# Kernel optimization log

Measured on AMD Instinct MI355X. Metric: run time of the kernel, lower is better.

Reference implementation:

```python
import jax, jax.numpy as jnp
import numpy as np

B, T, I, H = 4, 128, 32, 64


def setup_inputs() -> dict:
    key = jax.random.key(0)
    k1, k2, k3 = jax.random.split(key, 3)
    x = jax.random.normal(k1, (B, T, I), dtype=jnp.float32)
    carry = jnp.zeros((B, H), dtype=jnp.float32)  # RNNCell.initialize_carry uses zeros
    # lecun_normal-like input kernel (default_kernel_init)
    Wi = jax.random.normal(k2, (I, H), dtype=jnp.float32) / np.float32(np.sqrt(I))
    # orthogonal recurrent kernel init
    Wh, _ = jnp.linalg.qr(jax.random.normal(k3, (H, H), dtype=jnp.float32))
    b = jnp.zeros((H,), dtype=jnp.float32)
    return {"carry": carry, "x": x, "Wi": Wi, "Wh": Wh, "b": b}


def reference(carry, x, Wi, Wh, b):
    # Vanilla RNN step: a = tanh(x_t @ Wi + h @ Wh + b), scanned over time (axis 1).
    # Per step we also emit the analytic forward-mode Jacobian of the new state
    # w.r.t. (Wi, Wh, b, carry) -- exactly what jacfwd(fn, argnums=(0,1)) computes.
    Hh = Wh.shape[0]
    Bb = carry.shape[0]
    eyeH = jnp.eye(Hh, dtype=x.dtype)
    eyeB = jnp.eye(Bb, dtype=x.dtype)

    def step(h, x_t):
        a = jnp.tanh(x_t @ Wi + h @ Wh + b)  # (B, H)
        g = 1.0 - a * a                      # tanh' at preactivation, (B, H)
        # d a[b,j] / d Wi[i,k] = g[b,j] * x[b,i] * delta(j,k)  -> (B, H, I, H)
        J_Wi = jnp.einsum('bj,bi,jk->bjik', g, x_t, eyeH)
        # d a[b,j] / d Wh[m,k] = g[b,j] * h[b,m] * delta(j,k)  -> (B, H, H, H)
        J_Wh = jnp.einsum('bj,bm,jk->bjmk', g, h, eyeH)
        # d a[b,j] / d b[k]    = g[b,j] * delta(j,k)           -> (B, H, H)
        J_b = jnp.einsum('bj,jk->bjk', g, eyeH)
        # d a[b,j] / d h[c,m]  = g[b,j] * Wh[m,j] * delta(b,c) -> (B, H, B, H)
        J_h = jnp.einsum('bj,mj,bc->bjcm', g, Wh, eyeB)
        return a, (a, J_Wi, J_Wh, J_b, J_h)

    final_carry, ys = jax.lax.scan(step, carry, jnp.moveaxis(x, 1, 0))
    # out_axes=1: time axis goes to position 1 of every output leaf
    out, J_Wi, J_Wh, J_b, J_h = jax.tree.map(lambda y: jnp.moveaxis(y, 0, 1), ys)
    return final_carry, out, J_Wi, J_Wh, J_b, J_h
```

## Files before the change

kernel.cpp:

```cpp
#include <hip/hip_runtime.h>
#include <math.h>

#define OFF_OUT   256u
#define OFF_JWI   33024u
#define OFF_JWH   67141888u
#define OFF_JB    201359616u
#define OFF_JH    203456768u

typedef float f32x4 __attribute__((ext_vector_type(4)));

static __device__ __forceinline__ float tanh_fast(float x) {
    float t = __expf(2.0f * x);
    return 1.0f - 2.0f / (t + 1.0f);
}

static __device__ __forceinline__ void nt_store4(f32x4* p, float a, float b,
                                                 float c, float d) {
    f32x4 r = {a, b, c, d};
    __builtin_nontemporal_store(r, p);
}

__global__ __launch_bounds__(256) void xwi_kernel(
    const float* __restrict__ x, const float* __restrict__ Wi,
    const float* __restrict__ bias, float* __restrict__ u)
{
    const int tid = threadIdx.x;
    const int row = blockIdx.x * 4 + (tid >> 6);
    const int j = tid & 63;
    const float* xr = x + row * 32;
    float acc = bias[j];
#pragma unroll
    for (int i = 0; i < 32; ++i) acc = fmaf(xr[i], Wi[i * 64 + j], acc);
    u[row * 64 + j] = acc;
}

__global__ __launch_bounds__(64) void scan_kernel(
    const float* __restrict__ carry, const float* __restrict__ u,
    const float* __restrict__ Wh, float* __restrict__ out)
{
    const int b = blockIdx.x;
    const int j = threadIdx.x;
    float wcol[64];
#pragma unroll
    for (int m = 0; m < 64; ++m) wcol[m] = Wh[m * 64 + j];

    __shared__ float sh[64];
    sh[j] = carry[b * 64 + j];
    const float* ub = u + b * 128 * 64;
    float* ob = out + OFF_OUT + b * 128 * 64;
    float unext = ub[j];
    float a = 0.0f;
    __syncthreads();

    for (int t = 0; t < 128; ++t) {
        const float pre0 = unext;
        if (t < 127) unext = ub[(t + 1) * 64 + j];
        float a0 = 0.f, a1 = 0.f, a2 = 0.f, a3 = 0.f;
#pragma unroll
        for (int m = 0; m < 64; m += 4) {
            a0 = fmaf(sh[m + 0], wcol[m + 0], a0);
            a1 = fmaf(sh[m + 1], wcol[m + 1], a1);
            a2 = fmaf(sh[m + 2], wcol[m + 2], a2);
            a3 = fmaf(sh[m + 3], wcol[m + 3], a3);
        }
        a = tanh_fast(pre0 + (a0 + a1) + (a2 + a3));
        ob[t * 64 + j] = a;
        __syncthreads();
        sh[j] = a;
        __syncthreads();
    }
    out[b * 64 + j] = a;
}

__global__ __launch_bounds__(256) void fill_main(
    const float* __restrict__ carry, const float* __restrict__ x,
    float* __restrict__ out)
{
    __shared__ float smem[1024];
    const int tid = threadIdx.x;
    const unsigned blk = blockIdx.x;
    const float* __restrict__ outh = out + OFF_OUT;
    const unsigned rowq = tid >> 4;
    const unsigned k0 = (tid & 15u) * 4;

    if (blk < 1024u) {
        const unsigned bt = blk >> 1, jh = blk & 1u;
        if (tid < 32) {
            const float aa = outh[bt * 64 + jh * 32 + tid];
            smem[tid] = 1.0f - aa * aa;
            smem[32 + tid] = x[bt * 32 + tid];
        }
        __syncthreads();
        f32x4* dst = reinterpret_cast<f32x4*>(
            out + (size_t)OFF_JWI + (size_t)bt * 131072 + jh * 65536);
        const unsigned jbase = jh * 32;
#pragma unroll 2
        for (int it = 0; it < 64; ++it) {
            const unsigned R = it * 16 + rowq;
            const unsigned jloc = R >> 5, i = R & 31u;
            const float val = smem[jloc] * smem[32 + i];
            const unsigned d = (jbase + jloc) - k0;
            nt_store4(dst + it * 256 + tid,
                      (d == 0u) ? val : 0.f, (d == 1u) ? val : 0.f,
                      (d == 2u) ? val : 0.f, (d == 3u) ? val : 0.f);
        }
    } else if (blk < 3072u) {
        const unsigned idx = blk - 1024u;
        const unsigned bt = idx >> 2, jq = idx & 3u;
        const unsigned t = bt & 127u, bb = bt >> 7;
        if (tid < 16) {
            const float aa = outh[bt * 64 + jq * 16 + tid];
            smem[tid] = 1.0f - aa * aa;
        } else if (tid >= 64 && tid < 128) {
            const unsigned m = tid - 64;
            smem[64 + m] = (t == 0u) ? carry[bb * 64 + m]
                                     : outh[(bt - 1u) * 64 + m];
        }
        __syncthreads();
        f32x4* dst = reinterpret_cast<f32x4*>(
            out + (size_t)OFF_JWH + (size_t)bt * 262144 + jq * 65536);
        const unsigned jbase = jq * 16;
#pragma unroll 2
        for (int it = 0; it < 64; ++it) {
            const unsigned R = it * 16 + rowq;
            const unsigned jloc = R >> 6, m = R & 63u;
            const float val = smem[jloc] * smem[64 + m];
            const unsigned d = (jbase + jloc) - k0;
            nt_store4(dst + it * 256 + tid,
                      (d == 0u) ? val : 0.f, (d == 1u) ? val : 0.f,
                      (d == 2u) ? val : 0.f, (d == 3u) ? val : 0.f);
        }
    } else {
        const unsigned c = blk - 3072u;
        for (int p = tid; p < 1024; p += 256) {
            const float aa = outh[c * 1024 + p];
            smem[p] = 1.0f - aa * aa;
        }
        __syncthreads();
        f32x4* dst = reinterpret_cast<f32x4*>(
            out + (size_t)OFF_JB + (size_t)c * 65536);
#pragma unroll 2
        for (int it = 0; it < 64; ++it) {
            const unsigned R = it * 16 + rowq;
            const unsigned j = R & 63u;
            const float val = smem[R];
            const unsigned d = j - k0;
            nt_store4(dst + it * 256 + tid,
                      (d == 0u) ? val : 0.f, (d == 1u) ? val : 0.f,
                      (d == 2u) ? val : 0.f, (d == 3u) ? val : 0.f);
        }
    }
}

__global__ __launch_bounds__(256) void fill_jh(
    const float* __restrict__ Wh, float* __restrict__ out)
{
    __shared__ float whT[64 * 68];
    __shared__ float sg[256];
    const int tid = threadIdx.x;
    const unsigned q = blockIdx.x;
    const float* __restrict__ outh = out + OFF_OUT;

    for (int p = tid; p < 4096; p += 256) {
        const unsigned m = p >> 6, j = p & 63u;
        whT[j * 68 + m] = Wh[p];
    }
    {
        const unsigned s = tid >> 6, j = tid & 63u;
        const float aa = outh[(q * 4 + s) * 64 + j];
        sg[tid] = 1.0f - aa * aa;
    }
    __syncthreads();

    const unsigned m0 = (tid & 15u) * 4;
    f32x4* dst = reinterpret_cast<f32x4*>(out + (size_t)OFF_JH + (size_t)q * 65536);
#pragma unroll 2
    for (int it = 0; it < 64; ++it) {
        const unsigned R = it * 16 + (tid >> 4);
        const unsigned s = R >> 8;
        const unsigned j = (R >> 2) & 63u;
        const unsigned cc = R & 3u;
        const unsigned bb = (q * 4 + s) >> 7;
        if (cc == bb) {
            const float g = sg[s * 64 + j];
            const float* wrow = &whT[j * 68 + m0];
            nt_store4(dst + it * 256 + tid,
                      g * wrow[0], g * wrow[1], g * wrow[2], g * wrow[3]);
        } else {
            nt_store4(dst + it * 256 + tid, 0.f, 0.f, 0.f, 0.f);
        }
    }
}

extern "C" void kernel_launch(void* const* d_in, const int* in_sizes, int n_in,
                              void* d_out, int out_size, void* d_ws, size_t ws_size,
                              hipStream_t stream) {
    const float* carry = (const float*)d_in[0];
    const float* x     = (const float*)d_in[1];
    const float* Wi    = (const float*)d_in[2];
    const float* Wh    = (const float*)d_in[3];
    const float* bias  = (const float*)d_in[4];
    float* out = (float*)d_out;
    float* u = out + OFF_JB;

    xwi_kernel <<<128, 256, 0, stream>>>(x, Wi, bias, u);
    scan_kernel<<<4, 64, 0, stream>>>(carry, u, Wh, out);
    fill_main  <<<3104, 256, 0, stream>>>(carry, x, out);
    fill_jh    <<<128, 256, 0, stream>>>(Wh, out);
}
```

Baseline: 206.7 us.

## Overlap serial RNN scan with zero-filling of off-diagonal Jacobian blocks

The scan now runs in block 0 of a combined kernel, with one wavefront per batch row. It drops the per-step __syncthreads and relies on each wavefront executing in lockstep over its own shared-memory slice. The remaining blocks of that kernel write zeros to the halves of J_Wi, J_Wh and J_h that can never hold a nonzero, so that bandwidth-bound traffic overlaps the latency-bound recurrence. A second grid-stride kernel then writes only the diagonal-bearing parts of all four Jacobians, merging the former fill_main and fill_jh into one launch. The risk is that the barrier-free recurrence depends on wavefront-synchronous LDS ordering, and that the zero-fill now competes with the scan for the GPU.

```diff
diff --git a/kernel.cpp b/kernel.cpp
--- a/kernel.cpp
+++ b/kernel.cpp
@@ -14,12 +14,6 @@
     return 1.0f - 2.0f / (t + 1.0f);
 }
 
-static __device__ __forceinline__ void nt_store4(f32x4* p, float a, float b,
-                                                 float c, float d) {
-    f32x4 r = {a, b, c, d};
-    __builtin_nontemporal_store(r, p);
-}
-
 __global__ __launch_bounds__(256) void xwi_kernel(
     const float* __restrict__ x, const float* __restrict__ Wi,
     const float* __restrict__ bias, float* __restrict__ u)
@@ -34,161 +28,128 @@
     u[row * 64 + j] = acc;
 }
 
-__global__ __launch_bounds__(64) void scan_kernel(
+__global__ __launch_bounds__(256) void scan_zero_kernel(
     const float* __restrict__ carry, const float* __restrict__ u,
     const float* __restrict__ Wh, float* __restrict__ out)
 {
-    const int b = blockIdx.x;
-    const int j = threadIdx.x;
-    float wcol[64];
+    const int tid = threadIdx.x;
+    if (blockIdx.x == 0) {
+        const int w = tid >> 6, j = tid & 63;
+        float wcol[64];
 #pragma unroll
-    for (int m = 0; m < 64; ++m) wcol[m] = Wh[m * 64 + j];
-
-    __shared__ float sh[64];
-    sh[j] = carry[b * 64 + j];
-    const float* ub = u + b * 128 * 64;
-    float* ob = out + OFF_OUT + b * 128 * 64;
-    float unext = ub[j];
-    float a = 0.0f;
-    __syncthreads();
-
-    for (int t = 0; t < 128; ++t) {
-        const float pre0 = unext;
-        if (t < 127) unext = ub[(t + 1) * 64 + j];
-        float a0 = 0.f, a1 = 0.f, a2 = 0.f, a3 = 0.f;
+        for (int m = 0; m < 64; ++m) wcol[m] = Wh[m * 64 + j];
+        __shared__ __align__(16) float sh[256];
+        sh[tid] = carry[tid];
+        const float* ub = u + w * 8192;
+        float* ob = out + OFF_OUT + w * 8192;
+        const f32x4* shv = reinterpret_cast<const f32x4*>(sh + w * 64);
+        float unext = ub[j];
+        float a = 0.0f;
+        for (int t = 0; t < 128; ++t) {
+            const float pre = unext;
+            if (t < 127) unext = ub[(t + 1) * 64 + j];
+            float a0 = 0.f, a1 = 0.f, a2 = 0.f, a3 = 0.f;
 #pragma unroll
-        for (int m = 0; m < 64; m += 4) {
-            a0 = fmaf(sh[m + 0], wcol[m + 0], a0);
-            a1 = fmaf(sh[m + 1], wcol[m + 1], a1);
-            a2 = fmaf(sh[m + 2], wcol[m + 2], a2);
-            a3 = fmaf(sh[m + 3], wcol[m + 3], a3);
+            for (int mm = 0; mm < 16; ++mm) {
+                const f32x4 hv = shv[mm];
+                a0 = fmaf(hv.x, wcol[mm * 4 + 0], a0);
+                a1 = fmaf(hv.y, wcol[mm * 4 + 1], a1);
+                a2 = fmaf(hv.z, wcol[mm * 4 + 2], a2);
+                a3 = fmaf(hv.w, wcol[mm * 4 + 3], a3);
+            }
+            a = tanh_fast(pre + (a0 + a1) + (a2 + a3));
+            ob[t * 64 + j] = a;
+            sh[tid] = a;
         }
-        a = tanh_fast(pre0 + (a0 + a1) + (a2 + a3));
-        ob[t * 64 + j] = a;
-        __syncthreads();
-        sh[j] = a;
-        __syncthreads();
-    }
-    out[b * 64 + j] = a;
-}
-
-__global__ __launch_bounds__(256) void fill_main(
-    const float* __restrict__ carry, const float* __restrict__ x,
-    float* __restrict__ out)
-{
-    __shared__ float smem[1024];
-    const int tid = threadIdx.x;
-    const unsigned blk = blockIdx.x;
-    const float* __restrict__ outh = out + OFF_OUT;
-    const unsigned rowq = tid >> 4;
-    const unsigned k0 = (tid & 15u) * 4;
-
-    if (blk < 1024u) {
-        const unsigned bt = blk >> 1, jh = blk & 1u;
-        if (tid < 32) {
-            const float aa = outh[bt * 64 + jh * 32 + tid];
-            smem[tid] = 1.0f - aa * aa;
-            smem[32 + tid] = x[bt * 32 + tid];
-        }
-        __syncthreads();
-        f32x4* dst = reinterpret_cast<f32x4*>(
-            out + (size_t)OFF_JWI + (size_t)bt * 131072 + jh * 65536);
-        const unsigned jbase = jh * 32;
-#pragma unroll 2
-        for (int it = 0; it < 64; ++it) {
-            const unsigned R = it * 16 + rowq;
-            const unsigned jloc = R >> 5, i = R & 31u;
-            const float val = smem[jloc] * smem[32 + i];
-            const unsigned d = (jbase + jloc) - k0;
-            nt_store4(dst + it * 256 + tid,
-                      (d == 0u) ? val : 0.f, (d == 1u) ? val : 0.f,
-                      (d == 2u) ? val : 0.f, (d == 3u) ? val : 0.f);
-        }
-    } else if (blk < 3072u) {
-        const unsigned idx = blk - 1024u;
-        const unsigned bt = idx >> 2, jq = idx & 3u;
-        const unsigned t = bt & 127u, bb = bt >> 7;
-        if (tid < 16) {
-            const float aa = outh[bt * 64 + jq * 16 + tid];
-            smem[tid] = 1.0f - aa * aa;
-        } else if (tid >= 64 && tid < 128) {
-            const unsigned m = tid - 64;
-            smem[64 + m] = (t == 0u) ? carry[bb * 64 + m]
-                                     : outh[(bt - 1u) * 64 + m];
-        }
-        __syncthreads();
-        f32x4* dst = reinterpret_cast<f32x4*>(
-            out + (size_t)OFF_JWH + (size_t)bt * 262144 + jq * 65536);
-        const unsigned jbase = jq * 16;
-#pragma unroll 2
-        for (int it = 0; it < 64; ++it) {
-            const unsigned R = it * 16 + rowq;
-            const unsigned jloc = R >> 6, m = R & 63u;
-            const float val = smem[jloc] * smem[64 + m];
-            const unsigned d = (jbase + jloc) - k0;
-            nt_store4(dst + it * 256 + tid,
-                      (d == 0u) ? val : 0.f, (d == 1u) ? val : 0.f,
-                      (d == 2u) ? val : 0.f, (d == 3u) ? val : 0.f);
-        }
+        out[tid] = a;
     } else {
-        const unsigned c = blk - 3072u;
-        for (int p = tid; p < 1024; p += 256) {
-            const float aa = outh[c * 1024 + p];
-            smem[p] = 1.0f - aa * aa;
-        }
-        __syncthreads();
-        f32x4* dst = reinterpret_cast<f32x4*>(
-            out + (size_t)OFF_JB + (size_t)c * 65536);
-#pragma unroll 2
-        for (int it = 0; it < 64; ++it) {
-            const unsigned R = it * 16 + rowq;
-            const unsigned j = R & 63u;
-            const float val = smem[R];
-            const unsigned d = j - k0;
-            nt_store4(dst + it * 256 + tid,
-                      (d == 0u) ? val : 0.f, (d == 1u) ? val : 0.f,
-                      (d == 2u) ? val : 0.f, (d == 3u) ? val : 0.f);
+        const unsigned NW = (gridDim.x - 1u) * 4u;
+        const unsigned l = tid & 63u;
+        const f32x4 z = {0.f, 0.f, 0.f, 0.f};
+        for (unsigned uu = (blockIdx.x - 1u) * 4u + (tid >> 6);
+             uu < 425984u; uu += NW) {
+            unsigned addr;
+            if (uu < 131072u) {
+                const unsigned r0 = uu * 8u;
+                const unsigned j = (r0 >> 5) & 63u;
+                addr = OFF_JWI + r0 * 64u + ((j < 32u) ? 32u : 0u)
+                     + (l >> 3) * 64u + (l & 7u) * 4u;
+            } else if (uu < 393216u) {
+                const unsigned r0 = (uu - 131072u) * 8u;
+                const unsigned j = (r0 >> 6) & 63u;
+                addr = OFF_JWH + r0 * 64u + ((j < 32u) ? 32u : 0u)
+                     + (l >> 3) * 64u + (l & 7u) * 4u;
+            } else {
+                addr = OFF_JH + (uu - 393216u) * 256u + l * 4u;
+            }
+            __builtin_nontemporal_store(z, reinterpret_cast<f32x4*>(out + addr));
         }
     }
 }
 
-__global__ __launch_bounds__(256) void fill_jh(
+__global__ __launch_bounds__(256) void diag_fill_kernel(
+    const float* __restrict__ carry, const float* __restrict__ x,
     const float* __restrict__ Wh, float* __restrict__ out)
 {
-    __shared__ float whT[64 * 68];
-    __shared__ float sg[256];
     const int tid = threadIdx.x;
-    const unsigned q = blockIdx.x;
+    const unsigned NW = gridDim.x * 4u;
+    const unsigned l = tid & 63u;
     const float* __restrict__ outh = out + OFF_OUT;
 
-    for (int p = tid; p < 4096; p += 256) {
-        const unsigned m = p >> 6, j = p & 63u;
-        whT[j * 68 + m] = Wh[p];
-    }
-    {
-        const unsigned s = tid >> 6, j = tid & 63u;
-        const float aa = outh[(q * 4 + s) * 64 + j];
-        sg[tid] = 1.0f - aa * aa;
-    }
-    __syncthreads();
-
-    const unsigned m0 = (tid & 15u) * 4;
-    f32x4* dst = reinterpret_cast<f32x4*>(out + (size_t)OFF_JH + (size_t)q * 65536);
-#pragma unroll 2
-    for (int it = 0; it < 64; ++it) {
-        const unsigned R = it * 16 + (tid >> 4);
-        const unsigned s = R >> 8;
-        const unsigned j = (R >> 2) & 63u;
-        const unsigned cc = R & 3u;
-        const unsigned bb = (q * 4 + s) >> 7;
-        if (cc == bb) {
-            const float g = sg[s * 64 + j];
-            const float* wrow = &whT[j * 68 + m0];
-            nt_store4(dst + it * 256 + tid,
-                      g * wrow[0], g * wrow[1], g * wrow[2], g * wrow[3]);
+    for (unsigned uu = blockIdx.x * 4u + (tid >> 6); uu < 409600u; uu += NW) {
+        unsigned addr;
+        f32x4 r = {0.f, 0.f, 0.f, 0.f};
+        if (uu < 131072u) {
+            const unsigned r0 = uu * 8u;
+            const unsigned bt = r0 >> 11;
+            const unsigned j = (r0 >> 5) & 63u;
+            const float a = outh[bt * 64u + j];
+            const float g = 1.0f - a * a;
+            const unsigned i = (r0 + (l >> 3)) & 31u;
+            const float v = g * x[bt * 32u + i];
+            const unsigned d = (j & 31u) - (l & 7u) * 4u;
+            r.x = (d == 0u) ? v : 0.f; r.y = (d == 1u) ? v : 0.f;
+            r.z = (d == 2u) ? v : 0.f; r.w = (d == 3u) ? v : 0.f;
+            addr = OFF_JWI + r0 * 64u + ((j < 32u) ? 0u : 32u)
+                 + (l >> 3) * 64u + (l & 7u) * 4u;
+        } else if (uu < 393216u) {
+            const unsigned r0 = (uu - 131072u) * 8u;
+            const unsigned bt = r0 >> 12;
+            const unsigned j = (r0 >> 6) & 63u;
+            const unsigned t = bt & 127u, b = bt >> 7;
+            const float a = outh[bt * 64u + j];
+            const float g = 1.0f - a * a;
+            const unsigned m = (r0 + (l >> 3)) & 63u;
+            const float hv = (t == 0u) ? carry[b * 64u + m]
+                                       : outh[(bt - 1u) * 64u + m];
+            const float v = g * hv;
+            const unsigned d = (j & 31u) - (l & 7u) * 4u;
+            r.x = (d == 0u) ? v : 0.f; r.y = (d == 1u) ? v : 0.f;
+            r.z = (d == 2u) ? v : 0.f; r.w = (d == 3u) ? v : 0.f;
+            addr = OFF_JWH + r0 * 64u + ((j < 32u) ? 0u : 32u)
+                 + (l >> 3) * 64u + (l & 7u) * 4u;
+        } else if (uu < 401408u) {
+            const unsigned p = (uu - 393216u) * 4u + (l >> 4);
+            const unsigned j = p & 63u;
+            const float a = outh[p];
+            const float g = 1.0f - a * a;
+            const unsigned d = j - (l & 15u) * 4u;
+            r.x = (d == 0u) ? g : 0.f; r.y = (d == 1u) ? g : 0.f;
+            r.z = (d == 2u) ? g : 0.f; r.w = (d == 3u) ? g : 0.f;
+            addr = OFF_JB + p * 64u + (l & 15u) * 4u;
         } else {
-            nt_store4(dst + it * 256 + tid, 0.f, 0.f, 0.f, 0.f);
+            const unsigned p = (uu - 401408u) * 4u + (l >> 4);
+            const unsigned bt = p >> 6, j = p & 63u, b = bt >> 7;
+            const float a = outh[p];
+            const float g = 1.0f - a * a;
+            const unsigned k0 = (l & 15u) * 4u;
+            r.x = g * Wh[(k0 + 0u) * 64u + j];
+            r.y = g * Wh[(k0 + 1u) * 64u + j];
+            r.z = g * Wh[(k0 + 2u) * 64u + j];
+            r.w = g * Wh[(k0 + 3u) * 64u + j];
+            addr = OFF_JH + p * 256u + b * 64u + k0;
         }
+        __builtin_nontemporal_store(r, reinterpret_cast<f32x4*>(out + addr));
     }
 }
 
@@ -203,8 +164,7 @@
     float* out = (float*)d_out;
     float* u = out + OFF_JB;
 
-    xwi_kernel <<<128, 256, 0, stream>>>(x, Wi, bias, u);
-    scan_kernel<<<4, 64, 0, stream>>>(carry, u, Wh, out);
-    fill_main  <<<3104, 256, 0, stream>>>(carry, x, out);
-    fill_jh    <<<128, 256, 0, stream>>>(Wh, out);
+    xwi_kernel      <<<128, 256, 0, stream>>>(x, Wi, bias, u);
+    scan_zero_kernel<<<2048, 256, 0, stream>>>(carry, u, Wh, out);
+    diag_fill_kernel<<<2048, 256, 0, stream>>>(carry, x, Wh, out);
 }
```

Measured after the change: 184.4 us. -10.8%, faster.

## Merge fill kernels, stage scan inputs in LDS and drop scan barriers

Applied to the files above, without the earlier changes.

Merges the J_h fill into the main fill kernel, giving one launch and one grid that covers all Jacobian outputs, and moves the J_Wh blocks to the front of the grid. The scan kernel now preloads the whole per-batch preactivation sequence into LDS, keeps the input projection in the out buffer, reads the hidden state as vectors and removes both __syncthreads per step, relying on the 64-thread block being a single wavefront. This targets launch overhead and the barrier latency on the serial recurrence. Without barriers, correctness depends on lockstep wavefront execution, and the block-level fill needs more shared memory.

```diff
diff --git a/kernel.cpp b/kernel.cpp
--- a/kernel.cpp
+++ b/kernel.cpp
@@ -6,6 +6,7 @@
 #define OFF_JWH   67141888u
 #define OFF_JB    201359616u
 #define OFF_JH    203456768u
+#define OUT_TOTAL 211845376u
 
 typedef float f32x4 __attribute__((ext_vector_type(4)));
 
@@ -14,15 +15,9 @@
     return 1.0f - 2.0f / (t + 1.0f);
 }
 
-static __device__ __forceinline__ void nt_store4(f32x4* p, float a, float b,
-                                                 float c, float d) {
-    f32x4 r = {a, b, c, d};
-    __builtin_nontemporal_store(r, p);
-}
-
 __global__ __launch_bounds__(256) void xwi_kernel(
     const float* __restrict__ x, const float* __restrict__ Wi,
-    const float* __restrict__ bias, float* __restrict__ u)
+    const float* __restrict__ bias, float* __restrict__ out)
 {
     const int tid = threadIdx.x;
     const int row = blockIdx.x * 4 + (tid >> 6);
@@ -31,82 +26,60 @@
     float acc = bias[j];
 #pragma unroll
     for (int i = 0; i < 32; ++i) acc = fmaf(xr[i], Wi[i * 64 + j], acc);
-    u[row * 64 + j] = acc;
+    out[OFF_OUT + row * 64 + j] = acc;
 }
 
 __global__ __launch_bounds__(64) void scan_kernel(
-    const float* __restrict__ carry, const float* __restrict__ u,
-    const float* __restrict__ Wh, float* __restrict__ out)
+    const float* __restrict__ carry, const float* __restrict__ Wh,
+    float* __restrict__ out)
 {
     const int b = blockIdx.x;
     const int j = threadIdx.x;
+    __shared__ __align__(16) float uL[128 * 64];
+    __shared__ __align__(16) float sh[64];
+
     float wcol[64];
 #pragma unroll
     for (int m = 0; m < 64; ++m) wcol[m] = Wh[m * 64 + j];
 
-    __shared__ float sh[64];
+    float* ub = out + OFF_OUT + b * 8192;
+#pragma unroll 4
+    for (int p = j; p < 8192; p += 64) uL[p] = ub[p];
     sh[j] = carry[b * 64 + j];
-    const float* ub = u + b * 128 * 64;
-    float* ob = out + OFF_OUT + b * 128 * 64;
-    float unext = ub[j];
+
+    const f32x4* shv = reinterpret_cast<const f32x4*>(sh);
     float a = 0.0f;
-    __syncthreads();
-
     for (int t = 0; t < 128; ++t) {
-        const float pre0 = unext;
-        if (t < 127) unext = ub[(t + 1) * 64 + j];
+        const float pre = uL[t * 64 + j];
         float a0 = 0.f, a1 = 0.f, a2 = 0.f, a3 = 0.f;
 #pragma unroll
-        for (int m = 0; m < 64; m += 4) {
-            a0 = fmaf(sh[m + 0], wcol[m + 0], a0);
-            a1 = fmaf(sh[m + 1], wcol[m + 1], a1);
-            a2 = fmaf(sh[m + 2], wcol[m + 2], a2);
-            a3 = fmaf(sh[m + 3], wcol[m + 3], a3);
+        for (int mm = 0; mm < 16; ++mm) {
+            const f32x4 hv = shv[mm];
+            a0 = fmaf(hv.x, wcol[mm * 4 + 0], a0);
+            a1 = fmaf(hv.y, wcol[mm * 4 + 1], a1);
+            a2 = fmaf(hv.z, wcol[mm * 4 + 2], a2);
+            a3 = fmaf(hv.w, wcol[mm * 4 + 3], a3);
         }
-        a = tanh_fast(pre0 + (a0 + a1) + (a2 + a3));
-        ob[t * 64 + j] = a;
-        __syncthreads();
+        a = tanh_fast(pre + (a0 + a1) + (a2 + a3));
+        ub[t * 64 + j] = a;
         sh[j] = a;
-        __syncthreads();
     }
     out[b * 64 + j] = a;
 }
 
-__global__ __launch_bounds__(256) void fill_main(
+__global__ __launch_bounds__(256) void fill_kernel(
     const float* __restrict__ carry, const float* __restrict__ x,
-    float* __restrict__ out)
+    const float* __restrict__ Wh, float* __restrict__ out)
 {
-    __shared__ float smem[1024];
+    __shared__ float smem[4608];
     const int tid = threadIdx.x;
     const unsigned blk = blockIdx.x;
     const float* __restrict__ outh = out + OFF_OUT;
     const unsigned rowq = tid >> 4;
     const unsigned k0 = (tid & 15u) * 4;
 
-    if (blk < 1024u) {
-        const unsigned bt = blk >> 1, jh = blk & 1u;
-        if (tid < 32) {
-            const float aa = outh[bt * 64 + jh * 32 + tid];
-            smem[tid] = 1.0f - aa * aa;
-            smem[32 + tid] = x[bt * 32 + tid];
-        }
-        __syncthreads();
-        f32x4* dst = reinterpret_cast<f32x4*>(
-            out + (size_t)OFF_JWI + (size_t)bt * 131072 + jh * 65536);
-        const unsigned jbase = jh * 32;
-#pragma unroll 2
-        for (int it = 0; it < 64; ++it) {
-            const unsigned R = it * 16 + rowq;
-            const unsigned jloc = R >> 5, i = R & 31u;
-            const float val = smem[jloc] * smem[32 + i];
-            const unsigned d = (jbase + jloc) - k0;
-            nt_store4(dst + it * 256 + tid,
-                      (d == 0u) ? val : 0.f, (d == 1u) ? val : 0.f,
-                      (d == 2u) ? val : 0.f, (d == 3u) ? val : 0.f);
-        }
-    } else if (blk < 3072u) {
-        const unsigned idx = blk - 1024u;
-        const unsigned bt = idx >> 2, jq = idx & 3u;
+    if (blk < 2048u) {
+        const unsigned bt = blk >> 2, jq = blk & 3u;
         const unsigned t = bt & 127u, bb = bt >> 7;
         if (tid < 16) {
             const float aa = outh[bt * 64 + jq * 16 + tid];
@@ -126,11 +99,35 @@
             const unsigned jloc = R >> 6, m = R & 63u;
             const float val = smem[jloc] * smem[64 + m];
             const unsigned d = (jbase + jloc) - k0;
-            nt_store4(dst + it * 256 + tid,
-                      (d == 0u) ? val : 0.f, (d == 1u) ? val : 0.f,
-                      (d == 2u) ? val : 0.f, (d == 3u) ? val : 0.f);
+            f32x4 r;
+            r.x = (d == 0u) ? val : 0.f; r.y = (d == 1u) ? val : 0.f;
+            r.z = (d == 2u) ? val : 0.f; r.w = (d == 3u) ? val : 0.f;
+            __builtin_nontemporal_store(r, dst + it * 256 + tid);
         }
-    } else {
+    } else if (blk < 3072u) {
+        const unsigned idx = blk - 2048u;
+        const unsigned bt = idx >> 1, jh = idx & 1u;
+        if (tid < 32) {
+            const float aa = outh[bt * 64 + jh * 32 + tid];
+            smem[tid] = 1.0f - aa * aa;
+            smem[32 + tid] = x[bt * 32 + tid];
+        }
+        __syncthreads();
+        f32x4* dst = reinterpret_cast<f32x4*>(
+            out + (size_t)OFF_JWI + (size_t)bt * 131072 + jh * 65536);
+        const unsigned jbase = jh * 32;
+#pragma unroll 2
+        for (int it = 0; it < 64; ++it) {
+            const unsigned R = it * 16 + rowq;
+            const unsigned jloc = R >> 5, i = R & 31u;
+            const float val = smem[jloc] * smem[32 + i];
+            const unsigned d = (jbase + jloc) - k0;
+            f32x4 r;
+            r.x = (d == 0u) ? val : 0.f; r.y = (d == 1u) ? val : 0.f;
+            r.z = (d == 2u) ? val : 0.f; r.w = (d == 3u) ? val : 0.f;
+            __builtin_nontemporal_store(r, dst + it * 256 + tid);
+        }
+    } else if (blk < 3104u) {
         const unsigned c = blk - 3072u;
         for (int p = tid; p < 1024; p += 256) {
             const float aa = outh[c * 1024 + p];
@@ -145,49 +142,43 @@
             const unsigned j = R & 63u;
             const float val = smem[R];
             const unsigned d = j - k0;
-            nt_store4(dst + it * 256 + tid,
-                      (d == 0u) ? val : 0.f, (d == 1u) ? val : 0.f,
-                      (d == 2u) ? val : 0.f, (d == 3u) ? val : 0.f);
+            f32x4 r;
+            r.x = (d == 0u) ? val : 0.f; r.y = (d == 1u) ? val : 0.f;
+            r.z = (d == 2u) ? val : 0.f; r.w = (d == 3u) ? val : 0.f;
+            __builtin_nontemporal_store(r, dst + it * 256 + tid);
         }
-    }
-}
-
-__global__ __launch_bounds__(256) void fill_jh(
-    const float* __restrict__ Wh, float* __restrict__ out)
-{
-    __shared__ float whT[64 * 68];
-    __shared__ float sg[256];
-    const int tid = threadIdx.x;
-    const unsigned q = blockIdx.x;
-    const float* __restrict__ outh = out + OFF_OUT;
-
-    for (int p = tid; p < 4096; p += 256) {
-        const unsigned m = p >> 6, j = p & 63u;
-        whT[j * 68 + m] = Wh[p];
-    }
-    {
-        const unsigned s = tid >> 6, j = tid & 63u;
-        const float aa = outh[(q * 4 + s) * 64 + j];
-        sg[tid] = 1.0f - aa * aa;
-    }
-    __syncthreads();
-
-    const unsigned m0 = (tid & 15u) * 4;
-    f32x4* dst = reinterpret_cast<f32x4*>(out + (size_t)OFF_JH + (size_t)q * 65536);
+    } else {
+        const unsigned q = blk - 3104u;
+        float* whT = smem;
+        float* sg = smem + 4352;
+        for (int p = tid; p < 4096; p += 256) {
+            const unsigned m = p >> 6, j = p & 63u;
+            whT[j * 68 + m] = Wh[p];
+        }
+        {
+            const unsigned s = tid >> 6, j = tid & 63u;
+            const float aa = outh[(q * 4 + s) * 64 + j];
+            sg[tid] = 1.0f - aa * aa;
+        }
+        __syncthreads();
+        const unsigned m0 = (tid & 15u) * 4;
+        f32x4* dst = reinterpret_cast<f32x4*>(
+            out + (size_t)OFF_JH + (size_t)q * 65536);
 #pragma unroll 2
-    for (int it = 0; it < 64; ++it) {
-        const unsigned R = it * 16 + (tid >> 4);
-        const unsigned s = R >> 8;
-        const unsigned j = (R >> 2) & 63u;
-        const unsigned cc = R & 3u;
-        const unsigned bb = (q * 4 + s) >> 7;
-        if (cc == bb) {
-            const float g = sg[s * 64 + j];
-            const float* wrow = &whT[j * 68 + m0];
-            nt_store4(dst + it * 256 + tid,
-                      g * wrow[0], g * wrow[1], g * wrow[2], g * wrow[3]);
-        } else {
-            nt_store4(dst + it * 256 + tid, 0.f, 0.f, 0.f, 0.f);
+        for (int it = 0; it < 64; ++it) {
+            const unsigned R = it * 16 + rowq;
+            const unsigned s = R >> 8;
+            const unsigned j = (R >> 2) & 63u;
+            const unsigned cc = R & 3u;
+            const unsigned bb = (q * 4 + s) >> 7;
+            f32x4 r = {0.f, 0.f, 0.f, 0.f};
+            if (cc == bb) {
+                const float g = sg[s * 64 + j];
+                const float* wrow = &whT[j * 68 + m0];
+                r.x = g * wrow[0]; r.y = g * wrow[1];
+                r.z = g * wrow[2]; r.w = g * wrow[3];
+            }
+            __builtin_nontemporal_store(r, dst + it * 256 + tid);
         }
     }
 }
@@ -201,10 +192,8 @@
     const float* Wh    = (const float*)d_in[3];
     const float* bias  = (const float*)d_in[4];
     float* out = (float*)d_out;
-    float* u = out + OFF_JB;
 
-    xwi_kernel <<<128, 256, 0, stream>>>(x, Wi, bias, u);
-    scan_kernel<<<4, 64, 0, stream>>>(carry, u, Wh, out);
-    fill_main  <<<3104, 256, 0, stream>>>(carry, x, out);
-    fill_jh    <<<128, 256, 0, stream>>>(Wh, out);
+    xwi_kernel <<<128, 256, 0, stream>>>(x, Wi, bias, out);
+    scan_kernel<<<4, 64, 0, stream>>>(carry, Wh, out);
+    fill_kernel<<<3232, 256, 0, stream>>>(carry, x, Wh, out);
 }
```

After: 203.7 us. No clear change (-1.5%).
